# Optimization experiments

Hardware: AMD Instinct MI355X
Metric: run time of the kernel (lower is better)

Reference implementation:

```python
import jax, jax.numpy as jnp
import numpy as np

H = 2048          # hidden_size
NH = 16           # num_heads
HD = H // NH      # head_dim = 128
B, S = 2, 2048


def setup_inputs() -> dict:
    key = jax.random.key(0)
    ks = jax.random.split(key, 9)
    sc_h = 1.0 / np.sqrt(H)
    x = jax.random.normal(ks[0], (B, S, H), dtype=jnp.float32)
    # torch nn.Linear weights are [out_features, in_features]
    Wq = jax.random.uniform(ks[1], (H, H), jnp.float32, -sc_h, sc_h)
    bq = jax.random.uniform(ks[2], (H,), jnp.float32, -sc_h, sc_h)
    Wk = jax.random.uniform(ks[3], (HD, H), jnp.float32, -sc_h, sc_h)
    bk = jax.random.uniform(ks[4], (HD,), jnp.float32, -sc_h, sc_h)
    Wv = jax.random.uniform(ks[5], (HD, H), jnp.float32, -sc_h, sc_h)
    bv = jax.random.uniform(ks[6], (HD,), jnp.float32, -sc_h, sc_h)
    Wo = jax.random.uniform(ks[7], (H, H), jnp.float32, -sc_h, sc_h)
    bo = jax.random.uniform(ks[8], (H,), jnp.float32, -sc_h, sc_h)
    return {"x": x, "Wq": Wq, "bq": bq, "Wk": Wk, "bk": bk,
            "Wv": Wv, "bv": bv, "Wo": Wo, "bo": bo}


def reference(x, Wq, bq, Wk, bk, Wv, bv, Wo, bo):
    b, s, _ = x.shape
    q = (jnp.einsum('bsh,oh->bso', x, Wq) + bq).reshape(b, s, NH, HD)
    q = q.transpose(0, 2, 1, 3)                      # [b, nh, s, hd]
    k = jnp.einsum('bsh,dh->bsd', x, Wk) + bk        # [b, s, hd] single KV head
    v = jnp.einsum('bsh,dh->bsd', x, Wv) + bv
    # shared-K attention scores: broadcast single K head across query heads
    attn = jnp.einsum('bnsd,btd->bnst', q, k) / jnp.sqrt(jnp.float32(HD))
    attn = jax.nn.softmax(attn, axis=-1)
    out = jnp.einsum('bnst,btd->bnsd', attn, v)      # [b, nh, s, hd]
    out = out.transpose(0, 2, 1, 3).reshape(b, s, H)
    return jnp.einsum('bsh,oh->bso', out, Wo) + bo
```

## Files before the change

kernel.cpp:

```cpp
#include <hip/hip_runtime.h>
#include <hip/hip_bf16.h>

typedef unsigned short u16;
typedef __bf16 bf16x8 __attribute__((ext_vector_type(8)));
typedef float f32x4 __attribute__((ext_vector_type(4)));

#define AS1 __attribute__((address_space(1)))
#define AS3 __attribute__((address_space(3)))

__device__ __forceinline__ u16 f2bf(float f) {
  unsigned u = __builtin_bit_cast(unsigned, f);
  u += 0x7FFFu + ((u >> 16) & 1u);
  return (u16)(u >> 16);
}

__device__ __forceinline__ void gload_lds16(const void* g, void* l) {
  __builtin_amdgcn_global_load_lds((AS1 void*)g, (AS3 void*)l, 16, 0, 0);
}

__global__ __launch_bounds__(256)
void cvt_all(const float* __restrict__ x,
             const float* __restrict__ Wq, const float* __restrict__ Wk,
             const float* __restrict__ Wv, const float* __restrict__ Wo,
             const float* __restrict__ bq, const float* __restrict__ bk,
             const float* __restrict__ bv,
             u16* __restrict__ xb, u16* __restrict__ wqkv, u16* __restrict__ wo,
             float* __restrict__ bias_a, float qs) {
  const long NX = 1048576, NQ = 524288, NK = 32768, NV = 32768, NO = 524288;
  const long NW = NX + NQ + NK + NV + NO;
  long i = (long)blockIdx.x * 256 + threadIdx.x;
  if (i >= NW) {
    int t = (int)(i - NW);
    if (t < 2048) bias_a[t] = bq[t] * qs;
    else if (t < 2176) bias_a[t] = bk[t - 2048];
    else if (t < 2304) bias_a[t] = bv[t - 2176];
    return;
  }
  const float* src;
  u16* dst;
  float s = 1.f;
  if (i < NX) { src = x + i * 8; dst = xb + i * 8; }
  else if (i < NX + NQ) { long j = i - NX; src = Wq + j * 8; dst = wqkv + j * 8; s = qs; }
  else if (i < NX + NQ + NK) { long j = i - NX - NQ; src = Wk + j * 8; dst = wqkv + 2048l * 2048 + j * 8; }
  else if (i < NX + NQ + NK + NV) { long j = i - NX - NQ - NK; src = Wv + j * 8; dst = wqkv + 2176l * 2048 + j * 8; }
  else { long j = i - NX - NQ - NK - NV; src = Wo + j * 8; dst = wo + j * 8; }
  float4 a = *(const float4*)src;
  float4 b = *(const float4*)(src + 4);
  u16 t[8] = {f2bf(a.x * s), f2bf(a.y * s), f2bf(a.z * s), f2bf(a.w * s),
              f2bf(b.x * s), f2bf(b.y * s), f2bf(b.z * s), f2bf(b.w * s)};
  *(uint4*)dst = *(const uint4*)t;
}

template<int MODE>
__global__ __launch_bounds__(256)
void gemm_bt(const u16* __restrict__ A, const u16* __restrict__ B,
             const float* __restrict__ bias, void* __restrict__ C0,
             void* __restrict__ C1, void* __restrict__ C2,
             int M, int N, int K, float scale)
{
  __shared__ u16 As[128 * 64];
  __shared__ u16 Bs[128 * 64];
  const int tid = threadIdx.x;
  const int wave = tid >> 6, lane = tid & 63;
  const int g = lane >> 4, r = lane & 15;
  const int wrow = (wave >> 1) * 64, wcol = (wave & 1) * 64;

  const int gx = gridDim.x;
  int lin = blockIdx.y * gx + blockIdx.x;
  const int cpx = (gx * gridDim.y) >> 3;
  lin = (lin & 7) * cpx + (lin >> 3);
  const long tM = (long)(lin / gx) * 128, tN = (long)(lin % gx) * 128;

  const int srow = (tid * 16) >> 7;
  const int scol = (tid & 7) * 8;

  f32x4 acc[4][4] = {};
  char* As3 = (char*)As;
  char* Bs3 = (char*)Bs;

  for (int kt = 0; kt < K; kt += 64) {
    __syncthreads();
#pragma unroll
    for (int p = 0; p < 4; p++) {
      const int row = p * 32 + srow;
      const int sc = scol ^ ((row & 7) << 3);
      gload_lds16(A + (tM + row) * K + kt + sc, As3 + p * 4096 + tid * 16);
      gload_lds16(B + (tN + row) * K + kt + sc, Bs3 + p * 4096 + tid * 16);
    }
    __syncthreads();

#pragma unroll
    for (int kk = 0; kk < 2; kk++) {
      bf16x8 a[4], b[4];
#pragma unroll
      for (int m = 0; m < 4; m++) {
        const int ra = wrow + m * 16 + r;
        a[m] = *(const bf16x8*)(As + ra * 64 + ((kk * 32 + g * 8) ^ ((ra & 7) << 3)));
      }
#pragma unroll
      for (int n = 0; n < 4; n++) {
        const int rb = wcol + n * 16 + r;
        b[n] = *(const bf16x8*)(Bs + rb * 64 + ((kk * 32 + g * 8) ^ ((rb & 7) << 3)));
      }
#pragma unroll
      for (int m = 0; m < 4; m++)
#pragma unroll
        for (int n = 0; n < 4; n++)
          acc[m][n] = __builtin_amdgcn_mfma_f32_16x16x32_bf16(a[m], b[n], acc[m][n], 0, 0, 0);
    }
  }

#pragma unroll
  for (int m = 0; m < 4; m++) {
    const long row0 = tM + wrow + m * 16 + g * 4;
#pragma unroll
    for (int n = 0; n < 4; n++) {
      const long col = tN + wcol + n * 16 + r;
      const float bb = bias[col];
      if (MODE == 0) {
#pragma unroll
        for (int q = 0; q < 4; q++)
          ((float*)C0)[(row0 + q) * N + col] = (acc[m][n][q] + bb) * scale;
      } else {
        u16 vals[4];
#pragma unroll
        for (int q = 0; q < 4; q++) vals[q] = f2bf(acc[m][n][q] + bb);
        if (col < 2048) {
#pragma unroll
          for (int q = 0; q < 4; q++)
            ((u16*)C0)[(row0 + q) * 2048 + col] = vals[q];
        } else if (col < 2176) {
#pragma unroll
          for (int q = 0; q < 4; q++)
            ((u16*)C1)[(row0 + q) * 128 + (col - 2048)] = vals[q];
        } else {
          const long b2 = row0 >> 11;
          const long t0r = row0 & 2047;
          const int tl = (int)(t0r & 63);
          const int rbase = tl & 15, blk = tl >> 4;
          u16* vp = (u16*)C2 + (b2 * 128 + (col - 2176)) * 2048 + (t0r >> 6) * 64;
#pragma unroll
          for (int q = 0; q < 4; q++)
            vp[(rbase + q) * 4 + blk] = vals[q];
        }
      }
    }
  }
}

__global__ __launch_bounds__(512, 2)
void attn_mqa13(const u16* __restrict__ Q, const u16* __restrict__ Kb,
                const u16* __restrict__ VT, u16* __restrict__ O)
{
  constexpr int S = 2048;
  const int bid = blockIdx.x;
  const int qt = bid & 7;
  const int head = (bid >> 3) & 15;
  const int b = bid >> 7;
  const int tid = threadIdx.x;
  const int wave = tid >> 6, lane = tid & 63;
  const int g = lane >> 4, r = lane & 15;

  __shared__ u16 Ks[2][64 * 128];
  __shared__ u16 VTs[2][128 * 64];
  __shared__ u16 Ps[8][16 * 64];

  bf16x8 qf[2][4];
#pragma unroll
  for (int qb = 0; qb < 2; qb++) {
    const u16* qp = Q + (long)(b * S + qt * 256 + qb * 128 + wave * 16 + r) * 2048
                      + head * 128 + g * 8;
#pragma unroll
    for (int ks = 0; ks < 4; ks++) qf[qb][ks] = *(const bf16x8*)(qp + ks * 32);
  }

  f32x4 oacc[2][8] = {};
  float lsum[2][4] = {};
  char* psb = (char*)Ps[wave];

  auto stageK = [&](int buf, int t0) {
    char* dst = (char*)Ks[buf];
#pragma unroll
    for (int p = 0; p < 2; p++) {
      int D = p * 8192 + wave * 1024 + lane * 16;
      int row = D >> 8;
      int col2 = (D & 255) ^ ((row & 7) << 4);
      gload_lds16(Kb + ((long)b * S + t0 + row) * 128 + (col2 >> 1), dst + D);
    }
  };
  auto stageV = [&](int buf, int t0) {
    char* dst = (char*)VTs[buf];
#pragma unroll
    for (int p = 0; p < 2; p++) {
      int D = p * 8192 + wave * 1024 + lane * 16;
      int row = D >> 7;
      int colb = (D & 127) ^ ((row & 7) << 4);
      gload_lds16(VT + ((long)b * 128 + row) * 2048 + t0 + (colb >> 1), dst + D);
    }
  };

  stageK(0, 0);
  stageV(0, 0);
  __syncthreads();

  for (int t0 = 0; t0 < S; t0 += 64) {
    const int cur = (t0 >> 6) & 1;
    const bool nxt = (t0 + 64) < S;

    if (nxt) { stageK(cur ^ 1, t0 + 64); stageV(cur ^ 1, t0 + 64); }

    char* Ks3 = (char*)Ks[cur];
    f32x4 st[2][4] = {};
    __builtin_amdgcn_s_setprio(1);
#pragma unroll
    for (int ks = 0; ks < 4; ks++) {
#pragma unroll
      for (int nf = 0; nf < 4; nf++) {
        const int trow = nf * 16 + r;
        const int col2 = (ks * 64 + g * 16) ^ ((trow & 7) << 4);
        bf16x8 kf = *(const bf16x8*)(Ks3 + trow * 256 + col2);
        st[0][nf] = __builtin_amdgcn_mfma_f32_16x16x32_bf16(qf[0][ks], kf, st[0][nf], 0, 0, 0);
        st[1][nf] = __builtin_amdgcn_mfma_f32_16x16x32_bf16(qf[1][ks], kf, st[1][nf], 0, 0, 0);
      }
    }
    __builtin_amdgcn_s_setprio(0);

    char* Vs3 = (char*)VTs[cur];
    bf16x8 vreg[2][8];
#pragma unroll
    for (int qb = 0; qb < 2; qb++) {
#pragma unroll
      for (int q = 0; q < 4; q++) {
        const int prow = g * 4 + q;
        u16 pk[4];
#pragma unroll
        for (int nf = 0; nf < 4; nf++) {
          float p = __builtin_amdgcn_exp2f(st[qb][nf][q]);
          lsum[qb][q] += p;
          pk[nf] = __builtin_bit_cast(u16, (__bf16)p);
        }
        *(ushort4*)(psb + prow * 128 + ((r * 8) ^ ((prow & 7) << 4))) =
            *(const ushort4*)pk;
      }
      __builtin_amdgcn_s_setprio(1);
#pragma unroll
      for (int ks = 0; ks < 2; ks++) {
        bf16x8 pf = *(const bf16x8*)(psb + r * 128 +
                                     ((ks * 64 + g * 16) ^ ((r & 7) << 4)));
#pragma unroll
        for (int dn = 0; dn < 8; dn++) {
          if (qb == 0) {
            const int d = dn * 16 + r;
            vreg[ks][dn] = *(const bf16x8*)(Vs3 + d * 128 +
                                            ((ks * 64 + g * 16) ^ ((d & 7) << 4)));
          }
          oacc[qb][dn] = __builtin_amdgcn_mfma_f32_16x16x32_bf16(pf, vreg[ks][dn],
                                                                 oacc[qb][dn], 0, 0, 0);
        }
      }
      __builtin_amdgcn_s_setprio(0);
    }

    __syncthreads();
  }

#pragma unroll
  for (int off = 1; off < 16; off <<= 1)
#pragma unroll
    for (int qb = 0; qb < 2; qb++)
#pragma unroll
      for (int q = 0; q < 4; q++)
        lsum[qb][q] += __shfl_xor(lsum[qb][q], off);

#pragma unroll
  for (int qb = 0; qb < 2; qb++) {
#pragma unroll
    for (int q = 0; q < 4; q++) {
      const float inv = 1.f / lsum[qb][q];
      const long orow = (long)(b * S + qt * 256 + qb * 128 + wave * 16 + g * 4 + q);
#pragma unroll
      for (int dn = 0; dn < 8; dn++)
        O[orow * 2048 + head * 128 + dn * 16 + r] = f2bf(oacc[qb][dn][q] * inv);
    }
  }
}

extern "C" void kernel_launch(void* const* d_in, const int* in_sizes, int n_in,
                              void* d_out, int out_size, void* d_ws, size_t ws_size,
                              hipStream_t stream) {
  const float* x  = (const float*)d_in[0];
  const float* Wq = (const float*)d_in[1];
  const float* bq = (const float*)d_in[2];
  const float* Wk = (const float*)d_in[3];
  const float* bk = (const float*)d_in[4];
  const float* Wv = (const float*)d_in[5];
  const float* bv = (const float*)d_in[6];
  const float* Wo = (const float*)d_in[7];
  const float* bo = (const float*)d_in[8];
  float* out = (float*)d_out;

  char* ws = (char*)d_ws;
  u16* x_bf     = (u16*)(ws + (0ul  << 20));
  u16* q_bf     = (u16*)(ws + (16ul << 20));
  u16* wqkv_bf  = (u16*)(ws + (32ul << 20));
  u16* wo_bf    = (u16*)(ws + (42ul << 20));
  u16* k_bf     = (u16*)(ws + (50ul << 20));
  u16* vt_bf    = (u16*)(ws + (51ul << 20));
  u16* attn_bf  = (u16*)(ws + (52ul << 20));
  float* bias_a = (float*)(ws + (68ul << 20));

  const float QS = 0.12751744f;

  cvt_all<<<8457, 256, 0, stream>>>(x, Wq, Wk, Wv, Wo, bq, bk, bv,
                                    x_bf, wqkv_bf, wo_bf, bias_a, QS);

  gemm_bt<3><<<dim3(18, 32), 256, 0, stream>>>(
      x_bf, wqkv_bf, bias_a, q_bf, k_bf, vt_bf, 4096, 2304, 2048, 1.0f);
  attn_mqa13<<<256, 512, 0, stream>>>(q_bf, k_bf, vt_bf, attn_bf);
  gemm_bt<0><<<dim3(16, 32), 256, 0, stream>>>(
      attn_bf, wo_bf, bo, out, nullptr, nullptr, 4096, 2048, 2048, 1.0f);
}
```

Baseline: 190.6 us.

## Keep softmax probabilities in registers by transposing MFMA operands and permuting V layout

Swaps the A/B operands of both attention MFMAs so the score accumulator comes out transposed. Each lane can then pack its exp2 results directly into the bf16x8 B-operand for the PV MFMA, which removes the per-wave LDS round trip for P. The V^T layout written by the QKV GEMM epilogue is permuted to match the new key ordering, and that write becomes one vector store. Row sums now reduce with two shuffles instead of four, and outputs are written as 4-wide vectors. The risk is that the permutation of V rows must exactly match the MFMA register layout, or the results will be wrong.

Measured after the change: 215.0 us. 12.8% more time.

```diff
diff --git a/kernel.cpp b/kernel.cpp
--- a/kernel.cpp
+++ b/kernel.cpp
@@ -2,6 +2,7 @@
 #include <hip/hip_bf16.h>
 
 typedef unsigned short u16;
+typedef unsigned int u32;
 typedef __bf16 bf16x8 __attribute__((ext_vector_type(8)));
 typedef float f32x4 __attribute__((ext_vector_type(4)));
 
@@ -12,6 +13,10 @@
   unsigned u = __builtin_bit_cast(unsigned, f);
   u += 0x7FFFu + ((u >> 16) & 1u);
   return (u16)(u >> 16);
+}
+
+__device__ __forceinline__ u32 pack2bf(float a, float b) {
+  return (u32)f2bf(a) | ((u32)f2bf(b) << 16);
 }
 
 __device__ __forceinline__ void gload_lds16(const void* g, void* l) {
@@ -137,11 +142,9 @@
           const long b2 = row0 >> 11;
           const long t0r = row0 & 2047;
           const int tl = (int)(t0r & 63);
-          const int rbase = tl & 15, blk = tl >> 4;
+          const int base = ((tl >> 5) & 1) * 32 + ((tl >> 2) & 3) * 8 + ((tl >> 4) & 1) * 4;
           u16* vp = (u16*)C2 + (b2 * 128 + (col - 2176)) * 2048 + (t0r >> 6) * 64;
-#pragma unroll
-          for (int q = 0; q < 4; q++)
-            vp[(rbase + q) * 4 + blk] = vals[q];
+          *(ushort4*)(vp + base) = *(const ushort4*)vals;
         }
       }
     }
@@ -149,7 +152,7 @@
 }
 
 __global__ __launch_bounds__(512, 2)
-void attn_mqa13(const u16* __restrict__ Q, const u16* __restrict__ Kb,
+void attn_mqa14(const u16* __restrict__ Q, const u16* __restrict__ Kb,
                 const u16* __restrict__ VT, u16* __restrict__ O)
 {
   constexpr int S = 2048;
@@ -163,7 +166,6 @@
 
   __shared__ u16 Ks[2][64 * 128];
   __shared__ u16 VTs[2][128 * 64];
-  __shared__ u16 Ps[8][16 * 64];
 
   bf16x8 qf[2][4];
 #pragma unroll
@@ -175,8 +177,7 @@
   }
 
   f32x4 oacc[2][8] = {};
-  float lsum[2][4] = {};
-  char* psb = (char*)Ps[wave];
+  float lsum[2] = {0.f, 0.f};
 
   auto stageK = [&](int buf, int t0) {
     char* dst = (char*)Ks[buf];
@@ -219,8 +220,8 @@
         const int trow = nf * 16 + r;
         const int col2 = (ks * 64 + g * 16) ^ ((trow & 7) << 4);
         bf16x8 kf = *(const bf16x8*)(Ks3 + trow * 256 + col2);
-        st[0][nf] = __builtin_amdgcn_mfma_f32_16x16x32_bf16(qf[0][ks], kf, st[0][nf], 0, 0, 0);
-        st[1][nf] = __builtin_amdgcn_mfma_f32_16x16x32_bf16(qf[1][ks], kf, st[1][nf], 0, 0, 0);
+        st[0][nf] = __builtin_amdgcn_mfma_f32_16x16x32_bf16(kf, qf[0][ks], st[0][nf], 0, 0, 0);
+        st[1][nf] = __builtin_amdgcn_mfma_f32_16x16x32_bf16(kf, qf[1][ks], st[1][nf], 0, 0, 0);
       }
     }
     __builtin_amdgcn_s_setprio(0);
@@ -229,24 +230,26 @@
     bf16x8 vreg[2][8];
 #pragma unroll
     for (int qb = 0; qb < 2; qb++) {
-#pragma unroll
-      for (int q = 0; q < 4; q++) {
-        const int prow = g * 4 + q;
-        u16 pk[4];
-#pragma unroll
-        for (int nf = 0; nf < 4; nf++) {
-          float p = __builtin_amdgcn_exp2f(st[qb][nf][q]);
-          lsum[qb][q] += p;
-          pk[nf] = __builtin_bit_cast(u16, (__bf16)p);
+      bf16x8 pf[2];
+#pragma unroll
+      for (int ks = 0; ks < 2; ks++) {
+        float e0[4], e1[4];
+#pragma unroll
+        for (int reg = 0; reg < 4; reg++) {
+          e0[reg] = __builtin_amdgcn_exp2f(st[qb][ks * 2][reg]);
+          e1[reg] = __builtin_amdgcn_exp2f(st[qb][ks * 2 + 1][reg]);
+          lsum[qb] += e0[reg] + e1[reg];
         }
-        *(ushort4*)(psb + prow * 128 + ((r * 8) ^ ((prow & 7) << 4))) =
-            *(const ushort4*)pk;
+        uint4 w;
+        w.x = pack2bf(e0[0], e0[1]);
+        w.y = pack2bf(e0[2], e0[3]);
+        w.z = pack2bf(e1[0], e1[1]);
+        w.w = pack2bf(e1[2], e1[3]);
+        pf[ks] = __builtin_bit_cast(bf16x8, w);
       }
       __builtin_amdgcn_s_setprio(1);
 #pragma unroll
       for (int ks = 0; ks < 2; ks++) {
-        bf16x8 pf = *(const bf16x8*)(psb + r * 128 +
-                                     ((ks * 64 + g * 16) ^ ((r & 7) << 4)));
 #pragma unroll
         for (int dn = 0; dn < 8; dn++) {
           if (qb == 0) {
@@ -254,7 +257,7 @@
             vreg[ks][dn] = *(const bf16x8*)(Vs3 + d * 128 +
                                             ((ks * 64 + g * 16) ^ ((d & 7) << 4)));
           }
-          oacc[qb][dn] = __builtin_amdgcn_mfma_f32_16x16x32_bf16(pf, vreg[ks][dn],
+          oacc[qb][dn] = __builtin_amdgcn_mfma_f32_16x16x32_bf16(vreg[ks][dn], pf[ks],
                                                                  oacc[qb][dn], 0, 0, 0);
         }
       }
@@ -265,22 +268,22 @@
   }
 
 #pragma unroll
-  for (int off = 1; off < 16; off <<= 1)
-#pragma unroll
-    for (int qb = 0; qb < 2; qb++)
-#pragma unroll
-      for (int q = 0; q < 4; q++)
-        lsum[qb][q] += __shfl_xor(lsum[qb][q], off);
-
-#pragma unroll
   for (int qb = 0; qb < 2; qb++) {
-#pragma unroll
-    for (int q = 0; q < 4; q++) {
-      const float inv = 1.f / lsum[qb][q];
-      const long orow = (long)(b * S + qt * 256 + qb * 128 + wave * 16 + g * 4 + q);
-#pragma unroll
-      for (int dn = 0; dn < 8; dn++)
-        O[orow * 2048 + head * 128 + dn * 16 + r] = f2bf(oacc[qb][dn][q] * inv);
+    lsum[qb] += __shfl_xor(lsum[qb], 16);
+    lsum[qb] += __shfl_xor(lsum[qb], 32);
+  }
+
+#pragma unroll
+  for (int qb = 0; qb < 2; qb++) {
+    const float inv = 1.f / lsum[qb];
+    const long orow = (long)(b * S + qt * 256 + qb * 128 + wave * 16 + r);
+#pragma unroll
+    for (int dn = 0; dn < 8; dn++) {
+      u16 pk4[4];
+#pragma unroll
+      for (int reg = 0; reg < 4; reg++) pk4[reg] = f2bf(oacc[qb][dn][reg] * inv);
+      *(ushort4*)(O + orow * 2048 + head * 128 + dn * 16 + g * 4) =
+          *(const ushort4*)pk4;
     }
   }
 }
@@ -316,7 +319,7 @@
 
   gemm_bt<3><<<dim3(18, 32), 256, 0, stream>>>(
       x_bf, wqkv_bf, bias_a, q_bf, k_bf, vt_bf, 4096, 2304, 2048, 1.0f);
-  attn_mqa13<<<256, 512, 0, stream>>>(q_bf, k_bf, vt_bf, attn_bf);
+  attn_mqa14<<<256, 512, 0, stream>>>(q_bf, k_bf, vt_bf, attn_bf);
   gemm_bt<0><<<dim3(16, 32), 256, 0, stream>>>(
       attn_bf, wo_bf, bo, out, nullptr, nullptr, 4096, 2048, 2048, 1.0f);
 }
```
